# Kernel tuning notes

Measured on AMD Instinct MI355X. Metric: run time of the kernel, lower is better.

## Reference

```python
import jax, jax.numpy as jnp
import numpy as np

N_NODES = 20000
N_EDGES = 320000
N_RELS = 500
EMB = 256
D4 = EMB // 4
B = 32
GAMMA = 12.0
BN_EPS = 1e-5


def _linear(x, W, b):
    return x @ W.T + b


def _bn(x, g, b, m, v):
    # BatchNorm1d in eval mode with running stats
    return (x - m) * jax.lax.rsqrt(v + BN_EPS) * g + b


def _comp_layer(src, dst, h, e, WO, bO, WI, bI, WS, bS, bng, bnb, bnm, bnv):
    # CompGCNLayer: u_sub_e message + per-node mean over in-edges ('ho')
    # and, on the reversed graph, over out-edges ('hi'); nodes with no
    # incident edges get 0 (dgl mean semantics).
    n = h.shape[0]
    ones = jnp.ones(src.shape[0], h.dtype)
    deg_in = jnp.maximum(jax.ops.segment_sum(ones, dst, num_segments=n), 1.0)
    deg_out = jnp.maximum(jax.ops.segment_sum(ones, src, num_segments=n), 1.0)
    ho = jax.ops.segment_sum(h[src] - e, dst, num_segments=n) / deg_in[:, None]
    hi = jax.ops.segment_sum(h[dst] - e, src, num_segments=n) / deg_out[:, None]
    out = (_linear(ho, WO, bO) + _linear(hi, WI, bI) + _linear(h, WS, bS)) / 3.0
    return _bn(out, bng, bnb, bnm, bnv)


def _forward(node_embs, edge_embs, params, src, dst, e_vid, hids, rids, tids,
             is_update_g_embs, is_head_pred):
    (W_O1, b_O1, W_I1, b_I1, W_S1, b_S1, bn1_g, bn1_b, bn1_m, bn1_v, Wr1, br1,
     W_O2, b_O2, W_I2, b_I2, W_S2, b_S2, bn2_g, bn2_b, bn2_m, bn2_v, Wr2, br2) = params
    if is_update_g_embs:
        he = edge_embs[e_vid]                                   # [E, D]
        h1 = jnp.tanh(_comp_layer(src, dst, node_embs, he,
                                  W_O1, b_O1, W_I1, b_I1, W_S1, b_S1,
                                  bn1_g, bn1_b, bn1_m, bn1_v))  # [N, D/4]
        he1 = jnp.tanh(_linear(he, Wr1, br1))                   # [E, D/4]
        hn = jnp.tanh(_comp_layer(src, dst, h1, he1,
                                  W_O2, b_O2, W_I2, b_I2, W_S2, b_S2,
                                  bn2_g, bn2_b, bn2_m, bn2_v))  # [N, D]
    else:
        hn = node_embs
    heads = hn[hids]
    tails = hn[tids]
    rels = _linear(jax.nn.relu(_linear(edge_embs[rids], Wr1, br1)), Wr2, br2)
    b = hids.shape[0]
    n = hn.shape[0]
    # Faithful to torch repeat_interleave indexing in predict():
    # flat element k pairs query row k//C with candidate row k//B.
    cand_idx = (jnp.arange(b)[:, None] * n + jnp.arange(n)[None, :]) // b  # [B, N]
    cand = hn[cand_idx]                                                    # [B, N, D]
    if is_head_pred == 1:
        diff = cand + (rels - tails)[:, None, :]
    else:
        diff = (heads + rels)[:, None, :] - cand
    dist = jnp.sqrt(jnp.sum(diff * diff, axis=-1))  # p = norm = 2
    score = jax.nn.sigmoid(GAMMA - dist)
    return hn, score


def setup_inputs() -> dict:
    key = jax.random.key(0)
    ks = jax.random.split(key, 20)
    w = lambda k, shp: jax.random.normal(k, shp, jnp.float32) * 0.05
    inp = {
        "node_embs": jax.random.normal(ks[0], (N_NODES, EMB), jnp.float32),
        "edge_embs": jax.random.normal(ks[1], (N_RELS, EMB), jnp.float32),
        "W_O1": w(ks[2], (D4, EMB)), "b_O1": jnp.zeros((D4,), jnp.float32),
        "W_I1": w(ks[3], (D4, EMB)), "b_I1": jnp.zeros((D4,), jnp.float32),
        "W_S1": w(ks[4], (D4, EMB)), "b_S1": jnp.zeros((D4,), jnp.float32),
        "bn1_g": jnp.ones((D4,), jnp.float32), "bn1_b": jnp.zeros((D4,), jnp.float32),
        "bn1_m": jnp.zeros((D4,), jnp.float32), "bn1_v": jnp.ones((D4,), jnp.float32),
        "Wr1": w(ks[5], (D4, EMB)), "br1": jnp.zeros((D4,), jnp.float32),
        "W_O2": w(ks[6], (EMB, D4)), "b_O2": jnp.zeros((EMB,), jnp.float32),
        "W_I2": w(ks[7], (EMB, D4)), "b_I2": jnp.zeros((EMB,), jnp.float32),
        "W_S2": w(ks[8], (EMB, D4)), "b_S2": jnp.zeros((EMB,), jnp.float32),
        "bn2_g": jnp.ones((EMB,), jnp.float32), "bn2_b": jnp.zeros((EMB,), jnp.float32),
        "bn2_m": jnp.zeros((EMB,), jnp.float32), "bn2_v": jnp.ones((EMB,), jnp.float32),
        "Wr2": w(ks[9], (EMB, D4)), "br2": jnp.zeros((EMB,), jnp.float32),
        "src": jax.random.randint(ks[10], (N_EDGES,), 0, N_NODES, jnp.int32),
        "dst": jax.random.randint(ks[11], (N_EDGES,), 0, N_NODES, jnp.int32),
        "e_vid": jax.random.randint(ks[12], (N_EDGES,), 0, N_RELS, jnp.int32),
        "hids": jax.random.randint(ks[13], (B,), 0, N_NODES, jnp.int32),
        "rids": jax.random.randint(ks[14], (B,), 0, N_RELS, jnp.int32),
        "tids": jax.random.randint(ks[15], (B,), 0, N_NODES, jnp.int32),
        "is_update_g_embs": 1,
        "is_head_pred": 0,
    }
    return inp


def reference(node_embs, edge_embs,
              W_O1, b_O1, W_I1, b_I1, W_S1, b_S1, bn1_g, bn1_b, bn1_m, bn1_v,
              Wr1, br1,
              W_O2, b_O2, W_I2, b_I2, W_S2, b_S2, bn2_g, bn2_b, bn2_m, bn2_v,
              Wr2, br2,
              src, dst, e_vid, hids, rids, tids,
              is_update_g_embs, is_head_pred):
    params = (W_O1, b_O1, W_I1, b_I1, W_S1, b_S1, bn1_g, bn1_b, bn1_m, bn1_v,
              Wr1, br1,
              W_O2, b_O2, W_I2, b_I2, W_S2, b_S2, bn2_g, bn2_b, bn2_m, bn2_v,
              Wr2, br2)
    return _forward(node_embs, edge_embs, params, src, dst, e_vid,
                    hids, rids, tids, is_update_g_embs, is_head_pred)
```

## Files before the change

kernel.cpp:

```cpp
#include <hip/hip_runtime.h>
#include <math.h>

#define NN 20000
#define NE 320000
#define NR 500
#define EMBD 256
#define D4 64
#define BQ 32
#define TOT (2 * NN)
#define NB 40

#define NBLK_HIST 1250
#define NBLK_BN 448
#define NBLK_K1 (NBLK_HIST + NBLK_BN + 2 + BQ)

#define NBLK_GC1 939
#define NBLK_GE1 32
#define NBLK_MEGA (NBLK_GC1 + NBLK_GE1 + NBLK_HIST)

typedef __attribute__((ext_vector_type(8))) short bf16x8;
typedef __attribute__((ext_vector_type(4))) float f32x4;

__device__ __forceinline__ unsigned short f2bf(float x)
{
    unsigned int u = __float_as_uint(x);
    unsigned int r = (u + 0x7fffu + ((u >> 16) & 1u)) >> 16;
    return (unsigned short)r;
}

__device__ __forceinline__ float4 bf4tof4(uint2 u)
{
    float4 r;
    r.x = __uint_as_float((u.x & 0xFFFFu) << 16);
    r.y = __uint_as_float(u.x & 0xFFFF0000u);
    r.z = __uint_as_float((u.y & 0xFFFFu) << 16);
    r.w = __uint_as_float(u.y & 0xFFFF0000u);
    return r;
}

__global__ __launch_bounds__(256) void k_prep(
    const int* __restrict__ src, const int* __restrict__ dst,
    const int* __restrict__ evid, int* __restrict__ cnt, unsigned* __restrict__ rank2,
    const float* __restrict__ W_O1, const float* __restrict__ W_I1,
    const float* __restrict__ W_S1, const float* __restrict__ Wr1,
    const float* __restrict__ W_O2, const float* __restrict__ W_I2,
    const float* __restrict__ W_S2,
    unsigned short* __restrict__ Bn1, unsigned short* __restrict__ Bn2,
    const float* __restrict__ bO1, const float* __restrict__ bI1,
    const float* __restrict__ bS1,
    const float* __restrict__ g1, const float* __restrict__ bb1,
    const float* __restrict__ m1, const float* __restrict__ v1,
    const float* __restrict__ bO2, const float* __restrict__ bI2,
    const float* __restrict__ bS2,
    const float* __restrict__ g2, const float* __restrict__ bb2,
    const float* __restrict__ m2, const float* __restrict__ v2,
    float* __restrict__ s1, float* __restrict__ t1,
    float* __restrict__ s2, float* __restrict__ t2,
    const float* __restrict__ edge_embs,
    const float* __restrict__ br1, const float* __restrict__ br2,
    const float* __restrict__ Wr2full, const int* __restrict__ rids,
    float* __restrict__ rels)
{
    int b = blockIdx.x;
    if (b < NBLK_HIST) {
        int i = b * 256 + threadIdx.x;
        if (i < NE) {
            int r_in = atomicAdd(&cnt[dst[i]], 1);
            int r_out = atomicAdd(&cnt[NN + src[i]], 1);
            rank2[i] = (unsigned)r_in | ((unsigned)r_out << 16);
        }
        return;
    }
    b -= NBLK_HIST;
    if (b < NBLK_BN) {
        int id = b * 256 + threadIdx.x;
        if (id < 256 * 256) {
            int n = id >> 8, k = id & 255;
            float v;
            if (n < 64)       v = W_O1[n * 256 + k];
            else if (n < 128) v = W_I1[(n - 64) * 256 + k];
            else if (n < 192) v = W_S1[(n - 128) * 256 + k];
            else              v = Wr1[(n - 192) * 256 + k];
            Bn1[id] = f2bf(v);
        } else {
            int id2 = id - 256 * 256;
            if (id2 < 256 * 192) {
                int n = id2 / 192, k = id2 - n * 192;
                float v;
                if (k < 64)       v = W_O2[n * 64 + k];
                else if (k < 128) v = W_I2[n * 64 + (k - 64)];
                else              v = W_S2[n * 64 + (k - 128)];
                Bn2[id2] = f2bf(v);
            }
        }
        return;
    }
    b -= NBLK_BN;
    if (b < 2) {
        int i = b * 256 + threadIdx.x;
        if (i < 64) {
            float rsg = g1[i] / sqrtf(v1[i] + 1e-5f);
            s1[i] = rsg * (1.f / 3.f);
            t1[i] = ((bO1[i] + bI1[i] + bS1[i]) * (1.f / 3.f) - m1[i]) * rsg + bb1[i];
        } else if (i < 320) {
            int n = i - 64;
            float rsg = g2[n] / sqrtf(v2[n] + 1e-5f);
            s2[n] = rsg * (1.f / 3.f);
            t2[n] = ((bO2[n] + bI2[n] + bS2[n]) * (1.f / 3.f) - m2[n]) * rsg + bb2[n];
        }
        return;
    }
    {
        __shared__ float e_s[256];
        __shared__ float m_s[64];
        int rb = b - 2, o = threadIdx.x;
        int rid = rids[rb];
        e_s[o] = edge_embs[(size_t)rid * 256 + o];
        __syncthreads();
        if (o < 64) {
            float acc = br1[o];
            for (int k = 0; k < 256; ++k) acc = fmaf(e_s[k], Wr1[o * 256 + k], acc);
            m_s[o] = fmaxf(acc, 0.f);
        }
        __syncthreads();
        float r = br2[o];
        for (int jj = 0; jj < 64; ++jj) r = fmaf(m_s[jj], Wr2full[o * 64 + jj], r);
        rels[rb * 256 + o] = r;
    }
}


__global__ __launch_bounds__(256) void k_scanA(const int* __restrict__ cnt,
                                               int* __restrict__ bsum)
{
    __shared__ int lds[256];
    int t = threadIdx.x;
    int base = blockIdx.x * 1024 + t * 4;
    int s = 0;
    if (base + 3 < TOT) {
        int4 v = *(const int4*)(cnt + base);
        s = v.x + v.y + v.z + v.w;
    } else {
        for (int c = 0; c < 4; ++c) { int i = base + c; if (i < TOT) s += cnt[i]; }
    }
    lds[t] = s;
    __syncthreads();
    for (int d = 128; d > 0; d >>= 1) {
        if (t < d) lds[t] += lds[t + d];
        __syncthreads();
    }
    if (t == 0) bsum[blockIdx.x] = lds[0];
}

__global__ __launch_bounds__(64) void k_scanB(int* __restrict__ bsum)
{
    int t = threadIdx.x;
    int v = (t < NB) ? bsum[t] : 0;
#pragma unroll
    for (int d = 1; d < 64; d <<= 1) {
        int u = __shfl_up(v, d, 64);
        if (t >= d) v += u;
    }
    int ex = __shfl_up(v, 1, 64);
    if (t == 0) ex = 0;
    if (t < NB) bsum[t] = ex;
}

__global__ __launch_bounds__(256) void k_scanC(const int* __restrict__ cnt,
                                               const int* __restrict__ bsum,
                                               int* __restrict__ offc)
{
    __shared__ int lds[256];
    int t = threadIdx.x;
    int base = blockIdx.x * 1024 + t * 4;
    int e0 = 0, e1 = 0, e2 = 0, e3 = 0;
    if (base + 3 < TOT) {
        int4 v = *(const int4*)(cnt + base);
        e0 = v.x; e1 = v.y; e2 = v.z; e3 = v.w;
    } else {
        if (base + 0 < TOT) e0 = cnt[base + 0];
        if (base + 1 < TOT) e1 = cnt[base + 1];
        if (base + 2 < TOT) e2 = cnt[base + 2];
        if (base + 3 < TOT) e3 = cnt[base + 3];
    }
    int s = e0 + e1 + e2 + e3;
    lds[t] = s;
    __syncthreads();
    for (int d = 1; d < 256; d <<= 1) {
        int u = (t >= d) ? lds[t - d] : 0;
        __syncthreads();
        lds[t] += u;
        __syncthreads();
    }
    int run = lds[t] - s + bsum[blockIdx.x];
    if (base + 3 < TOT) {
        int4 o = make_int4(run, run + e0, run + e0 + e1, run + e0 + e1 + e2);
        *(int4*)(offc + base) = o;
    } else {
        int r = run;
        if (base + 0 < TOT) { offc[base + 0] = r; r += e0; }
        if (base + 1 < TOT) { offc[base + 1] = r; r += e1; }
        if (base + 2 < TOT) { offc[base + 2] = r; r += e2; }
        if (base + 3 < TOT) { offc[base + 3] = r; r += e3; }
    }
    if (blockIdx.x == 0 && t == 0) offc[TOT] = 2 * NE;
}

__device__ __forceinline__ void gemm_dev(
    unsigned short* As, unsigned short* Bs,
    const void* __restrict__ Av, int aBf16, int M, int K, int lda,
    const unsigned short* __restrict__ Bn,
    void* __restrict__ C, int ldc, int mode,
    const float* __restrict__ sv, const float* __restrict__ tv,
    const float* __restrict__ node_embs, const int* __restrict__ flag,
    int m0, int n0)
{
    const int t = threadIdx.x;
    const int lane = t & 63, wave = t >> 6;
    const int wr = wave >> 1, wc = wave & 1;
    const int lrow = lane & 15, lkg = lane >> 4;

    f32x4 acc[2][2] = {};

    for (int kb = 0; kb < K; kb += 64) {
        if (aBf16) {
            const unsigned short* A = (const unsigned short*)Av;
#pragma unroll
            for (int it = 0; it < 2; ++it) {
                int idx = t + it * 256;
                int ko = idx & 7;
                int row = idx >> 3;
                int gm = m0 + row;
                uint4 a = make_uint4(0u, 0u, 0u, 0u);
                if (gm < M) a = *(const uint4*)(A + (size_t)gm * lda + kb + 8 * ko);
                *(uint4*)&As[row * 72 + 8 * ko] = a;
            }
        } else {
            const float* A = (const float*)Av;
#pragma unroll
            for (int it = 0; it < 4; ++it) {
                int idx = t + it * 256;
                int kq = idx & 15;
                int row = idx >> 4;
                int gm = m0 + row;
                float4 a = make_float4(0.f, 0.f, 0.f, 0.f);
                if (gm < M) a = *(const float4*)(A + (size_t)gm * lda + kb + 4 * kq);
                unsigned int p0 = (unsigned int)f2bf(a.x) | ((unsigned int)f2bf(a.y) << 16);
                unsigned int p1 = (unsigned int)f2bf(a.z) | ((unsigned int)f2bf(a.w) << 16);
                *(uint2*)&As[row * 72 + 4 * kq] = make_uint2(p0, p1);
            }
        }
#pragma unroll
        for (int it = 0; it < 2; ++it) {
            int idx = t + it * 256;
            int ko = idx & 7;
            int row = idx >> 3;
            uint4 b = *(const uint4*)(Bn + (size_t)(n0 + row) * K + kb + 8 * ko);
            *(uint4*)&Bs[row * 72 + 8 * ko] = b;
        }
        __syncthreads();
#pragma unroll
        for (int ks = 0; ks < 2; ++ks) {
            int k0 = ks * 32 + lkg * 8;
            bf16x8 af0 = *(const bf16x8*)&As[(wr * 32 + lrow) * 72 + k0];
            bf16x8 af1 = *(const bf16x8*)&As[(wr * 32 + 16 + lrow) * 72 + k0];
            bf16x8 bf0 = *(const bf16x8*)&Bs[(wc * 32 + lrow) * 72 + k0];
            bf16x8 bf1 = *(const bf16x8*)&Bs[(wc * 32 + 16 + lrow) * 72 + k0];
            acc[0][0] = __builtin_amdgcn_mfma_f32_16x16x32_bf16(af0, bf0, acc[0][0], 0, 0, 0);
            acc[0][1] = __builtin_amdgcn_mfma_f32_16x16x32_bf16(af0, bf1, acc[0][1], 0, 0, 0);
            acc[1][0] = __builtin_amdgcn_mfma_f32_16x16x32_bf16(af1, bf0, acc[1][0], 0, 0, 0);
            acc[1][1] = __builtin_amdgcn_mfma_f32_16x16x32_bf16(af1, bf1, acc[1][1], 0, 0, 0);
        }
        __syncthreads();
    }

#pragma unroll
    for (int m = 0; m < 2; ++m) {
#pragma unroll
        for (int r = 0; r < 4; ++r) {
            int gm = m0 + wr * 32 + m * 16 + lkg * 4 + r;
            if (gm >= M) continue;
#pragma unroll
            for (int n = 0; n < 2; ++n) {
                int gn = n0 + wc * 32 + n * 16 + lrow;
                float v = acc[m][n][r];
                if (mode == 0) {
                    ((unsigned short*)C)[(size_t)gm * ldc + gn] = f2bf(v);
                } else if (mode == 1) {
                    float val = (gn >= 192) ? tanhf(v + sv[gn - 192]) : v;
                    ((unsigned short*)C)[(size_t)gm * ldc + gn] = f2bf(val);
                } else {
                    float val = tanhf(v * sv[gn] + tv[gn]);
                    if (flag[0] == 0) val = node_embs[(size_t)gm * EMBD + gn];
                    ((float*)C)[(size_t)gm * EMBD + gn] = val;
                }
            }
        }
    }
}

__global__ __launch_bounds__(256) void gemm_mfma(
    const void* __restrict__ A, int aBf16, int M, int K, int lda,
    const unsigned short* __restrict__ Bn,
    void* __restrict__ C, int ldc, int mode,
    const float* __restrict__ sv, const float* __restrict__ tv,
    const float* __restrict__ node_embs, const int* __restrict__ flag)
{
    __shared__ unsigned short As[64 * 72];
    __shared__ unsigned short Bs[64 * 72];
    gemm_dev(As, Bs, A, aBf16, M, K, lda, Bn, C, ldc, mode, sv, tv, node_embs, flag,
             blockIdx.x * 64, blockIdx.y * 64);
}

__global__ __launch_bounds__(256) void k_mega(
    const float* __restrict__ node_embs, const float* __restrict__ edge_embs,
    const unsigned short* __restrict__ Bn1,
    unsigned short* __restrict__ C1b, unsigned short* __restrict__ E1b,
    const float* __restrict__ br1,
    const int* __restrict__ src, const int* __restrict__ dst,
    const int* __restrict__ evid, const unsigned* __restrict__ rank2,
    const int* __restrict__ offc, unsigned* __restrict__ R)
{
    __shared__ unsigned short As[64 * 72];
    __shared__ unsigned short Bs[64 * 72];
    int bid = blockIdx.x;
    if (bid < NBLK_GC1) {
        gemm_dev(As, Bs, node_embs, 0, NN, 256, 256, Bn1, C1b, 192, 0,
                 nullptr, nullptr, nullptr, nullptr,
                 (bid % 313) * 64, (bid / 313) * 64);
    } else if (bid < NBLK_GC1 + NBLK_GE1) {
        int b2 = bid - NBLK_GC1;
        gemm_dev(As, Bs, edge_embs, 0, NR, 256, 256, Bn1, E1b, 256, 1,
                 br1, nullptr, nullptr, nullptr,
                 (b2 % 8) * 64, (b2 / 8) * 64);
    } else {
        int e = (bid - NBLK_GC1 - NBLK_GE1) * 256 + threadIdx.x;
        if (e < NE) {
            int s = src[e], d = dst[e];
            unsigned rv = (unsigned)evid[e] << 15;
            unsigned rk = rank2[e];
            R[offc[d] + (rk & 0xFFFFu)] = (unsigned)s | rv;
            R[offc[NN + s] + (rk >> 16)] = (unsigned)d | rv;
        }
    }
}


__device__ __forceinline__ void gather_quad(
    const unsigned* __restrict__ R, int r0, int r1, int g, int q,
    const unsigned short* __restrict__ TAB, int ldt, int toff,
    const unsigned short* __restrict__ ETAB, int eoff,
    float4& acc)
{
    int lane = g * 16 + q;
    int cnt = r1 - r0;
    for (int base = 0; base < cnt; base += 64) {
        int rem = cnt - base; if (rem > 64) rem = 64;
        unsigned rec = 0u;
        if (lane < rem) rec = R[r0 + base + lane];
        int i = 0;
        for (; 4 * i + 15 < rem; i += 4) {
            unsigned ra = __shfl(rec, 4 * i + g, 64);
            unsigned rb = __shfl(rec, 4 * i + 4 + g, 64);
            unsigned rc = __shfl(rec, 4 * i + 8 + g, 64);
            unsigned rd = __shfl(rec, 4 * i + 12 + g, 64);
            uint2 ua0 = *(const uint2*)(TAB + (size_t)(ra & 0x7FFFu) * ldt + toff + 4 * q);
            uint2 ue0 = *(const uint2*)(ETAB + (size_t)(ra >> 15) * 256 + eoff + 4 * q);
            uint2 ua1 = *(const uint2*)(TAB + (size_t)(rb & 0x7FFFu) * ldt + toff + 4 * q);
            uint2 ue1 = *(const uint2*)(ETAB + (size_t)(rb >> 15) * 256 + eoff + 4 * q);
            uint2 ua2 = *(const uint2*)(TAB + (size_t)(rc & 0x7FFFu) * ldt + toff + 4 * q);
            uint2 ue2 = *(const uint2*)(ETAB + (size_t)(rc >> 15) * 256 + eoff + 4 * q);
            uint2 ua3 = *(const uint2*)(TAB + (size_t)(rd & 0x7FFFu) * ldt + toff + 4 * q);
            uint2 ue3 = *(const uint2*)(ETAB + (size_t)(rd >> 15) * 256 + eoff + 4 * q);
            float4 a0 = bf4tof4(ua0), e0 = bf4tof4(ue0);
            float4 a1 = bf4tof4(ua1), e1 = bf4tof4(ue1);
            float4 a2 = bf4tof4(ua2), e2 = bf4tof4(ue2);
            float4 a3 = bf4tof4(ua3), e3 = bf4tof4(ue3);
            acc.x += (a0.x - e0.x) + (a1.x - e1.x) + (a2.x - e2.x) + (a3.x - e3.x);
            acc.y += (a0.y - e0.y) + (a1.y - e1.y) + (a2.y - e2.y) + (a3.y - e3.y);
            acc.z += (a0.z - e0.z) + (a1.z - e1.z) + (a2.z - e2.z) + (a3.z - e3.z);
            acc.w += (a0.w - e0.w) + (a1.w - e1.w) + (a2.w - e2.w) + (a3.w - e3.w);
        }
        for (; 4 * i < rem; ++i) {
            int idx = 4 * i + g;
            unsigned rr = __shfl(rec, idx < rem ? idx : 0, 64);
            if (idx < rem) {
                uint2 ua = *(const uint2*)(TAB + (size_t)(rr & 0x7FFFu) * ldt + toff + 4 * q);
                uint2 ue = *(const uint2*)(ETAB + (size_t)(rr >> 15) * 256 + eoff + 4 * q);
                float4 a = bf4tof4(ua), e = bf4tof4(ue);
                acc.x += a.x - e.x; acc.y += a.y - e.y;
                acc.z += a.z - e.z; acc.w += a.w - e.w;
            }
        }
    }
}

__device__ __forceinline__ void xreduce(float4& v)
{
    v.x += __shfl_xor(v.x, 16, 64); v.y += __shfl_xor(v.y, 16, 64);
    v.z += __shfl_xor(v.z, 16, 64); v.w += __shfl_xor(v.w, 16, 64);
    v.x += __shfl_xor(v.x, 32, 64); v.y += __shfl_xor(v.y, 32, 64);
    v.z += __shfl_xor(v.z, 32, 64); v.w += __shfl_xor(v.w, 32, 64);
}

__device__ __forceinline__ uint2 packbf4(float4 o)
{
    return make_uint2((unsigned)f2bf(o.x) | ((unsigned)f2bf(o.y) << 16),
                      (unsigned)f2bf(o.z) | ((unsigned)f2bf(o.w) << 16));
}

__global__ __launch_bounds__(256) void k_gather1(
    const int* __restrict__ offc, const unsigned* __restrict__ R,
    const unsigned short* __restrict__ C1b, const unsigned short* __restrict__ E1b,
    const float* __restrict__ s1, const float* __restrict__ t1,
    unsigned short* __restrict__ A2b)
{
    int n = blockIdx.x * 4 + (threadIdx.x >> 6);
    if (n >= NN) return;
    int lane = threadIdx.x & 63, g = lane >> 4, q = lane & 15;
    int b0 = offc[n], b1 = offc[n + 1];
    int c0 = offc[NN + n], c1 = offc[NN + n + 1];
    float di = 1.f / fmaxf((float)(b1 - b0), 1.f);
    float dh = 1.f / fmaxf((float)(c1 - c0), 1.f);
    float4 accO = make_float4(0.f, 0.f, 0.f, 0.f);
    float4 accI = make_float4(0.f, 0.f, 0.f, 0.f);
    gather_quad(R, b0, b1, g, q, C1b, 192, 0, E1b, 0, accO);
    gather_quad(R, c0, c1, g, q, C1b, 192, 64, E1b, 64, accI);
    xreduce(accO);
    xreduce(accI);
    if (g == 0) {
        float4 hs = bf4tof4(*(const uint2*)(C1b + (size_t)n * 192 + 128 + 4 * q));
        float4 sv = *(const float4*)(s1 + 4 * q);
        float4 tv = *(const float4*)(t1 + 4 * q);
        float4 o;
        o.x = tanhf((accO.x * di + accI.x * dh + hs.x) * sv.x + tv.x);
        o.y = tanhf((accO.y * di + accI.y * dh + hs.y) * sv.y + tv.y);
        o.z = tanhf((accO.z * di + accI.z * dh + hs.z) * sv.z + tv.z);
        o.w = tanhf((accO.w * di + accI.w * dh + hs.w) * sv.w + tv.w);
        *(uint2*)(A2b + (size_t)n * 192 + 128 + 4 * q) = packbf4(o);
    }
}

__global__ __launch_bounds__(256) void k_gather2(
    const int* __restrict__ offc, const unsigned* __restrict__ R,
    const unsigned short* __restrict__ A2r, const unsigned short* __restrict__ E1b,
    unsigned short* __restrict__ A2w)
{
    int n = blockIdx.x * 4 + (threadIdx.x >> 6);
    if (n >= NN) return;
    int lane = threadIdx.x & 63, g = lane >> 4, q = lane & 15;
    int b0 = offc[n], b1 = offc[n + 1];
    int c0 = offc[NN + n], c1 = offc[NN + n + 1];
    float di = 1.f / fmaxf((float)(b1 - b0), 1.f);
    float dh = 1.f / fmaxf((float)(c1 - c0), 1.f);
    float4 accO = make_float4(0.f, 0.f, 0.f, 0.f);
    float4 accI = make_float4(0.f, 0.f, 0.f, 0.f);
    gather_quad(R, b0, b1, g, q, A2r, 192, 128, E1b, 192, accO);
    gather_quad(R, c0, c1, g, q, A2r, 192, 128, E1b, 192, accI);
    xreduce(accO);
    xreduce(accI);
    if (g == 0) {
        float4 o0, o1;
        o0.x = accO.x * di; o0.y = accO.y * di; o0.z = accO.z * di; o0.w = accO.w * di;
        o1.x = accI.x * dh; o1.y = accI.y * dh; o1.z = accI.z * dh; o1.w = accI.w * dh;
        *(uint2*)(A2w + (size_t)n * 192 + 4 * q) = packbf4(o0);
        *(uint2*)(A2w + (size_t)n * 192 + 64 + 4 * q) = packbf4(o1);
    }
}

__global__ __launch_bounds__(256) void k_tvec(
    const float* __restrict__ rels, const float* __restrict__ hn,
    const int* __restrict__ hids, const int* __restrict__ tids,
    const int* __restrict__ is_head, float* __restrict__ tvec)
{
    int b = blockIdx.x, o = threadIdx.x;
    int ih = is_head[0];
    int nid = ih ? tids[b] : hids[b];
    float r = rels[b * 256 + o];
    float hv = hn[(size_t)nid * 256 + o];
    tvec[b * 256 + o] = ih ? (hv - r) : (hv + r);
}

__global__ __launch_bounds__(256) void k_score(
    const float* __restrict__ hn, const float* __restrict__ tvec,
    float* __restrict__ score)
{
    int p = blockIdx.x * 4 + (threadIdx.x >> 6);
    if (p >= BQ * (NN / BQ)) return;
    int l = threadIdx.x & 63;
    int b = p / (NN / BQ);
    int j = p - b * (NN / BQ);
    int idx = (b * NN + 32 * j) / BQ;
    float ssum = 0.f;
#pragma unroll
    for (int q = 0; q < 4; ++q) {
        float df = hn[(size_t)idx * 256 + l + 64 * q] - tvec[b * 256 + l + 64 * q];
        ssum = fmaf(df, df, ssum);
    }
#pragma unroll
    for (int off = 32; off >= 1; off >>= 1) ssum += __shfl_xor(ssum, off, 64);
    float dist = sqrtf(ssum);
    float sc = 1.f / (1.f + expf(dist - 12.f));
    if (l < 32) score[(size_t)b * NN + 32 * j + l] = sc;
}

extern "C" void kernel_launch(void* const* d_in, const int* in_sizes, int n_in,
                              void* d_out, int out_size, void* d_ws, size_t ws_size,
                              hipStream_t stream)
{
    const float* node_embs = (const float*)d_in[0];
    const float* edge_embs = (const float*)d_in[1];
    const float* W_O1 = (const float*)d_in[2];  const float* b_O1 = (const float*)d_in[3];
    const float* W_I1 = (const float*)d_in[4];  const float* b_I1 = (const float*)d_in[5];
    const float* W_S1 = (const float*)d_in[6];  const float* b_S1 = (const float*)d_in[7];
    const float* bn1_g = (const float*)d_in[8]; const float* bn1_b = (const float*)d_in[9];
    const float* bn1_m = (const float*)d_in[10];const float* bn1_v = (const float*)d_in[11];
    const float* Wr1 = (const float*)d_in[12];  const float* br1 = (const float*)d_in[13];
    const float* W_O2 = (const float*)d_in[14]; const float* b_O2 = (const float*)d_in[15];
    const float* W_I2 = (const float*)d_in[16]; const float* b_I2 = (const float*)d_in[17];
    const float* W_S2 = (const float*)d_in[18]; const float* b_S2 = (const float*)d_in[19];
    const float* bn2_g = (const float*)d_in[20];const float* bn2_b = (const float*)d_in[21];
    const float* bn2_m = (const float*)d_in[22];const float* bn2_v = (const float*)d_in[23];
    const float* Wr2 = (const float*)d_in[24];  const float* br2 = (const float*)d_in[25];
    const int* src = (const int*)d_in[26];
    const int* dst = (const int*)d_in[27];
    const int* evid = (const int*)d_in[28];
    const int* hids = (const int*)d_in[29];
    const int* rids = (const int*)d_in[30];
    const int* tids = (const int*)d_in[31];
    const int* upd = (const int*)d_in[32];
    const int* ihead = (const int*)d_in[33];

    unsigned short* C1b = (unsigned short*)d_ws;
    unsigned short* A2b = C1b + 3840000;
    unsigned short* E1b = A2b + 3840000;
    unsigned short* Bn1 = E1b + 128000;
    unsigned short* Bn2 = Bn1 + 65536;

    float* s1   = (float*)(Bn2 + 49152);
    float* t1   = s1 + 64;
    float* s2   = t1 + 64;
    float* t2   = s2 + 256;
    float* rels = t2 + 256;
    float* tvec = rels + 8192;

    unsigned* R     = (unsigned*)(tvec + 8192);
    unsigned* rank2 = R + 2 * NE;
    int* cnt    = (int*)(rank2 + NE);
    int* offc   = cnt + TOT;
    int* bsum   = offc + TOT + 1;

    float* hn    = (float*)d_out;
    float* score = hn + (size_t)NN * EMBD;

    hipMemsetAsync(cnt, 0, (size_t)TOT * 4, stream);

    k_prep<<<NBLK_K1, 256, 0, stream>>>(
        src, dst, evid, cnt, rank2,
        W_O1, W_I1, W_S1, Wr1, W_O2, W_I2, W_S2, Bn1, Bn2,
        b_O1, b_I1, b_S1, bn1_g, bn1_b, bn1_m, bn1_v,
        b_O2, b_I2, b_S2, bn2_g, bn2_b, bn2_m, bn2_v,
        s1, t1, s2, t2,
        edge_embs, br1, br2, Wr2, rids, rels);

    k_scanA<<<NB, 256, 0, stream>>>(cnt, bsum);
    k_scanB<<<1, 64, 0, stream>>>(bsum);
    k_scanC<<<NB, 256, 0, stream>>>(cnt, bsum, offc);

    k_mega<<<NBLK_MEGA, 256, 0, stream>>>(node_embs, edge_embs, Bn1,
                                          C1b, E1b, br1, src, dst, evid, rank2, offc, R);

    k_gather1<<<NN / 4, 256, 0, stream>>>(offc, R, C1b, E1b, s1, t1, A2b);
    k_gather2<<<NN / 4, 256, 0, stream>>>(offc, R, A2b, E1b, A2b);

    gemm_mfma<<<dim3(313, 4), 256, 0, stream>>>(A2b, 1, NN, 192, 192, Bn2,
                                                hn, 256, 2, s2, t2, node_embs, upd);

    k_tvec<<<BQ, 256, 0, stream>>>(rels, hn, hids, tids, ihead, tvec);
    k_score<<<(BQ * (NN / BQ)) / 4, 256, 0, stream>>>(hn, tvec, score);
}
```

Baseline: 143.2 us.

## Privatize edge histogram into 8 partitions and repack CSR per bin

The degree histogram now uses 8 private count arrays chosen by block index, which cuts atomic contention on shared bins. The scan is extended to produce per-partition offsets plus merged per-bin offsets. A new repack kernel copies the partitioned edge lists into one contiguous CSR array for the gather kernels. The scatter phase of k_mega is reordered to run first, and k_tvec is fused into k_score. The cost is an extra kernel, larger scans over 8x the bins, and a serial per-thread copy loop in the repack.

```diff
diff --git a/kernel.cpp b/kernel.cpp
--- a/kernel.cpp
+++ b/kernel.cpp
@@ -8,7 +8,10 @@
 #define D4 64
 #define BQ 32
 #define TOT (2 * NN)
-#define NB 40
+#define NPART 8
+#define TOT2 (NPART * TOT)
+#define NBP 313
+#define NBB 40
 
 #define NBLK_HIST 1250
 #define NBLK_BN 448
@@ -16,7 +19,7 @@
 
 #define NBLK_GC1 939
 #define NBLK_GE1 32
-#define NBLK_MEGA (NBLK_GC1 + NBLK_GE1 + NBLK_HIST)
+#define NBLK_MEGA (NBLK_HIST + NBLK_GC1 + NBLK_GE1)
 
 typedef __attribute__((ext_vector_type(8))) short bf16x8;
 typedef __attribute__((ext_vector_type(4))) float f32x4;
@@ -40,7 +43,7 @@
 
 __global__ __launch_bounds__(256) void k_prep(
     const int* __restrict__ src, const int* __restrict__ dst,
-    const int* __restrict__ evid, int* __restrict__ cnt, unsigned* __restrict__ rank2,
+    int* __restrict__ cnt2, unsigned* __restrict__ rank2,
     const float* __restrict__ W_O1, const float* __restrict__ W_I1,
     const float* __restrict__ W_S1, const float* __restrict__ Wr1,
     const float* __restrict__ W_O2, const float* __restrict__ W_I2,
@@ -64,9 +67,10 @@
     int b = blockIdx.x;
     if (b < NBLK_HIST) {
         int i = b * 256 + threadIdx.x;
+        int base = (b & (NPART - 1)) * TOT;
         if (i < NE) {
-            int r_in = atomicAdd(&cnt[dst[i]], 1);
-            int r_out = atomicAdd(&cnt[NN + src[i]], 1);
+            int r_in = atomicAdd(&cnt2[base + dst[i]], 1);
+            int r_out = atomicAdd(&cnt2[base + NN + src[i]], 1);
             rank2[i] = (unsigned)r_in | ((unsigned)r_out << 16);
         }
         return;
@@ -130,18 +134,31 @@
 }
 
 
-__global__ __launch_bounds__(256) void k_scanA(const int* __restrict__ cnt,
-                                               int* __restrict__ bsum)
+__global__ __launch_bounds__(256) void k_scanA(const int* __restrict__ cnt2,
+                                               int* __restrict__ bsum,
+                                               int* __restrict__ bsum2)
 {
     __shared__ int lds[256];
     int t = threadIdx.x;
-    int base = blockIdx.x * 1024 + t * 4;
+    int bid = blockIdx.x;
     int s = 0;
-    if (base + 3 < TOT) {
-        int4 v = *(const int4*)(cnt + base);
-        s = v.x + v.y + v.z + v.w;
+    if (bid < NBP) {
+        int base = bid * 1024 + t * 4;
+        if (base + 3 < TOT2) {
+            int4 v = *(const int4*)(cnt2 + base);
+            s = v.x + v.y + v.z + v.w;
+        } else {
+            for (int c = 0; c < 4; ++c) { int i = base + c; if (i < TOT2) s += cnt2[i]; }
+        }
     } else {
-        for (int c = 0; c < 4; ++c) { int i = base + c; if (i < TOT) s += cnt[i]; }
+        int base = (bid - NBP) * 1024 + t * 4;
+        for (int c = 0; c < 4; ++c) {
+            int bin = base + c;
+            if (bin < TOT) {
+#pragma unroll
+                for (int p = 0; p < NPART; ++p) s += cnt2[p * TOT + bin];
+            }
+        }
     }
     lds[t] = s;
     __syncthreads();
@@ -149,39 +166,66 @@
         if (t < d) lds[t] += lds[t + d];
         __syncthreads();
     }
-    if (t == 0) bsum[blockIdx.x] = lds[0];
-}
-
-__global__ __launch_bounds__(64) void k_scanB(int* __restrict__ bsum)
+    if (t == 0) {
+        if (bid < NBP) bsum[bid] = lds[0];
+        else bsum2[bid - NBP] = lds[0];
+    }
+}
+
+__global__ __launch_bounds__(64) void k_scanB(int* __restrict__ bsum, int* __restrict__ bsum2)
 {
     int t = threadIdx.x;
-    int v = (t < NB) ? bsum[t] : 0;
-#pragma unroll
-    for (int d = 1; d < 64; d <<= 1) {
-        int u = __shfl_up(v, d, 64);
-        if (t >= d) v += u;
-    }
-    int ex = __shfl_up(v, 1, 64);
-    if (t == 0) ex = 0;
-    if (t < NB) bsum[t] = ex;
-}
-
-__global__ __launch_bounds__(256) void k_scanC(const int* __restrict__ cnt,
+    int* arr = blockIdx.x ? bsum2 : bsum;
+    int nb = blockIdx.x ? NBB : NBP;
+    int carry = 0;
+    for (int c = 0; c < nb; c += 64) {
+        int i = c + t;
+        int v = (i < nb) ? arr[i] : 0;
+        int vin = v;
+#pragma unroll
+        for (int d = 1; d < 64; d <<= 1) {
+            int u = __shfl_up(v, d, 64);
+            if (t >= d) v += u;
+        }
+        if (i < nb) arr[i] = (v - vin) + carry;
+        carry += __shfl(v, 63, 64);
+    }
+}
+
+__global__ __launch_bounds__(256) void k_scanC(const int* __restrict__ cnt2,
                                                const int* __restrict__ bsum,
-                                               int* __restrict__ offc)
+                                               const int* __restrict__ bsum2,
+                                               int* __restrict__ offc2,
+                                               int* __restrict__ off_bin)
 {
     __shared__ int lds[256];
     int t = threadIdx.x;
-    int base = blockIdx.x * 1024 + t * 4;
+    int bid = blockIdx.x;
     int e0 = 0, e1 = 0, e2 = 0, e3 = 0;
-    if (base + 3 < TOT) {
-        int4 v = *(const int4*)(cnt + base);
-        e0 = v.x; e1 = v.y; e2 = v.z; e3 = v.w;
+    if (bid < NBP) {
+        int base = bid * 1024 + t * 4;
+        if (base + 3 < TOT2) {
+            int4 v = *(const int4*)(cnt2 + base);
+            e0 = v.x; e1 = v.y; e2 = v.z; e3 = v.w;
+        } else {
+            if (base + 0 < TOT2) e0 = cnt2[base + 0];
+            if (base + 1 < TOT2) e1 = cnt2[base + 1];
+            if (base + 2 < TOT2) e2 = cnt2[base + 2];
+            if (base + 3 < TOT2) e3 = cnt2[base + 3];
+        }
     } else {
-        if (base + 0 < TOT) e0 = cnt[base + 0];
-        if (base + 1 < TOT) e1 = cnt[base + 1];
-        if (base + 2 < TOT) e2 = cnt[base + 2];
-        if (base + 3 < TOT) e3 = cnt[base + 3];
+        int base = (bid - NBP) * 1024 + t * 4;
+        int es[4] = {0, 0, 0, 0};
+        for (int c = 0; c < 4; ++c) {
+            int bin = base + c;
+            if (bin < TOT) {
+                int acc = 0;
+#pragma unroll
+                for (int p = 0; p < NPART; ++p) acc += cnt2[p * TOT + bin];
+                es[c] = acc;
+            }
+        }
+        e0 = es[0]; e1 = es[1]; e2 = es[2]; e3 = es[3];
     }
     int s = e0 + e1 + e2 + e3;
     lds[t] = s;
@@ -192,18 +236,30 @@
         lds[t] += u;
         __syncthreads();
     }
-    int run = lds[t] - s + bsum[blockIdx.x];
-    if (base + 3 < TOT) {
-        int4 o = make_int4(run, run + e0, run + e0 + e1, run + e0 + e1 + e2);
-        *(int4*)(offc + base) = o;
+    if (bid < NBP) {
+        int base = bid * 1024 + t * 4;
+        int run = lds[t] - s + bsum[bid];
+        if (base + 3 < TOT2) {
+            int4 o = make_int4(run, run + e0, run + e0 + e1, run + e0 + e1 + e2);
+            *(int4*)(offc2 + base) = o;
+        } else {
+            int r = run;
+            if (base + 0 < TOT2) { offc2[base + 0] = r; r += e0; }
+            if (base + 1 < TOT2) { offc2[base + 1] = r; r += e1; }
+            if (base + 2 < TOT2) { offc2[base + 2] = r; r += e2; }
+            if (base + 3 < TOT2) { offc2[base + 3] = r; r += e3; }
+        }
+        if (bid == 0 && t == 0) offc2[TOT2] = 2 * NE;
     } else {
+        int base = (bid - NBP) * 1024 + t * 4;
+        int run = lds[t] - s + bsum2[bid - NBP];
         int r = run;
-        if (base + 0 < TOT) { offc[base + 0] = r; r += e0; }
-        if (base + 1 < TOT) { offc[base + 1] = r; r += e1; }
-        if (base + 2 < TOT) { offc[base + 2] = r; r += e2; }
-        if (base + 3 < TOT) { offc[base + 3] = r; r += e3; }
-    }
-    if (blockIdx.x == 0 && t == 0) offc[TOT] = 2 * NE;
+        if (base + 0 < TOT) { off_bin[base + 0] = r; r += e0; }
+        if (base + 1 < TOT) { off_bin[base + 1] = r; r += e1; }
+        if (base + 2 < TOT) { off_bin[base + 2] = r; r += e2; }
+        if (base + 3 < TOT) { off_bin[base + 3] = r; r += e3; }
+        if (bid == NBP && t == 0) off_bin[TOT] = 2 * NE;
+    }
 }
 
 __device__ __forceinline__ void gemm_dev(
@@ -319,29 +375,47 @@
     const float* __restrict__ br1,
     const int* __restrict__ src, const int* __restrict__ dst,
     const int* __restrict__ evid, const unsigned* __restrict__ rank2,
-    const int* __restrict__ offc, unsigned* __restrict__ R)
+    const int* __restrict__ offc2, unsigned* __restrict__ R)
 {
     __shared__ unsigned short As[64 * 72];
     __shared__ unsigned short Bs[64 * 72];
     int bid = blockIdx.x;
-    if (bid < NBLK_GC1) {
-        gemm_dev(As, Bs, node_embs, 0, NN, 256, 256, Bn1, C1b, 192, 0,
-                 nullptr, nullptr, nullptr, nullptr,
-                 (bid % 313) * 64, (bid / 313) * 64);
-    } else if (bid < NBLK_GC1 + NBLK_GE1) {
-        int b2 = bid - NBLK_GC1;
-        gemm_dev(As, Bs, edge_embs, 0, NR, 256, 256, Bn1, E1b, 256, 1,
-                 br1, nullptr, nullptr, nullptr,
-                 (b2 % 8) * 64, (b2 / 8) * 64);
-    } else {
-        int e = (bid - NBLK_GC1 - NBLK_GE1) * 256 + threadIdx.x;
+    if (bid < NBLK_HIST) {
+        int e = bid * 256 + threadIdx.x;
         if (e < NE) {
+            int base = (bid & (NPART - 1)) * TOT;
             int s = src[e], d = dst[e];
             unsigned rv = (unsigned)evid[e] << 15;
             unsigned rk = rank2[e];
-            R[offc[d] + (rk & 0xFFFFu)] = (unsigned)s | rv;
-            R[offc[NN + s] + (rk >> 16)] = (unsigned)d | rv;
-        }
+            R[offc2[base + d] + (rk & 0xFFFFu)] = (unsigned)s | rv;
+            R[offc2[base + NN + s] + (rk >> 16)] = (unsigned)d | rv;
+        }
+        return;
+    }
+    int b2 = bid - NBLK_HIST;
+    if (b2 < NBLK_GC1) {
+        gemm_dev(As, Bs, node_embs, 0, NN, 256, 256, Bn1, C1b, 192, 0,
+                 nullptr, nullptr, nullptr, nullptr,
+                 (b2 % 313) * 64, (b2 / 313) * 64);
+    } else {
+        int b3 = b2 - NBLK_GC1;
+        gemm_dev(As, Bs, edge_embs, 0, NR, 256, 256, Bn1, E1b, 256, 1,
+                 br1, nullptr, nullptr, nullptr,
+                 (b3 % 8) * 64, (b3 / 8) * 64);
+    }
+}
+
+__global__ void k_repack(const int* __restrict__ offc2, const int* __restrict__ off_bin,
+                         const unsigned* __restrict__ R, unsigned* __restrict__ R2)
+{
+    int bin = blockIdx.x * 256 + threadIdx.x;
+    if (bin >= TOT) return;
+    int d = off_bin[bin];
+#pragma unroll
+    for (int p = 0; p < NPART; ++p) {
+        int s = offc2[p * TOT + bin];
+        int e = offc2[p * TOT + bin + 1];
+        for (int i = s; i < e; ++i) R2[d++] = R[i];
     }
 }
 
@@ -410,7 +484,7 @@
 }
 
 __global__ __launch_bounds__(256) void k_gather1(
-    const int* __restrict__ offc, const unsigned* __restrict__ R,
+    const int* __restrict__ off_bin, const unsigned* __restrict__ R2,
     const unsigned short* __restrict__ C1b, const unsigned short* __restrict__ E1b,
     const float* __restrict__ s1, const float* __restrict__ t1,
     unsigned short* __restrict__ A2b)
@@ -418,14 +492,14 @@
     int n = blockIdx.x * 4 + (threadIdx.x >> 6);
     if (n >= NN) return;
     int lane = threadIdx.x & 63, g = lane >> 4, q = lane & 15;
-    int b0 = offc[n], b1 = offc[n + 1];
-    int c0 = offc[NN + n], c1 = offc[NN + n + 1];
+    int b0 = off_bin[n], b1 = off_bin[n + 1];
+    int c0 = off_bin[NN + n], c1 = off_bin[NN + n + 1];
     float di = 1.f / fmaxf((float)(b1 - b0), 1.f);
     float dh = 1.f / fmaxf((float)(c1 - c0), 1.f);
     float4 accO = make_float4(0.f, 0.f, 0.f, 0.f);
     float4 accI = make_float4(0.f, 0.f, 0.f, 0.f);
-    gather_quad(R, b0, b1, g, q, C1b, 192, 0, E1b, 0, accO);
-    gather_quad(R, c0, c1, g, q, C1b, 192, 64, E1b, 64, accI);
+    gather_quad(R2, b0, b1, g, q, C1b, 192, 0, E1b, 0, accO);
+    gather_quad(R2, c0, c1, g, q, C1b, 192, 64, E1b, 64, accI);
     xreduce(accO);
     xreduce(accI);
     if (g == 0) {
@@ -442,21 +516,21 @@
 }
 
 __global__ __launch_bounds__(256) void k_gather2(
-    const int* __restrict__ offc, const unsigned* __restrict__ R,
+    const int* __restrict__ off_bin, const unsigned* __restrict__ R2,
     const unsigned short* __restrict__ A2r, const unsigned short* __restrict__ E1b,
     unsigned short* __restrict__ A2w)
 {
     int n = blockIdx.x * 4 + (threadIdx.x >> 6);
     if (n >= NN) return;
     int lane = threadIdx.x & 63, g = lane >> 4, q = lane & 15;
-    int b0 = offc[n], b1 = offc[n + 1];
-    int c0 = offc[NN + n], c1 = offc[NN + n + 1];
+    int b0 = off_bin[n], b1 = off_bin[n + 1];
+    int c0 = off_bin[NN + n], c1 = off_bin[NN + n + 1];
     float di = 1.f / fmaxf((float)(b1 - b0), 1.f);
     float dh = 1.f / fmaxf((float)(c1 - c0), 1.f);
     float4 accO = make_float4(0.f, 0.f, 0.f, 0.f);
     float4 accI = make_float4(0.f, 0.f, 0.f, 0.f);
-    gather_quad(R, b0, b1, g, q, A2r, 192, 128, E1b, 192, accO);
-    gather_quad(R, c0, c1, g, q, A2r, 192, 128, E1b, 192, accI);
+    gather_quad(R2, b0, b1, g, q, A2r, 192, 128, E1b, 192, accO);
+    gather_quad(R2, c0, c1, g, q, A2r, 192, 128, E1b, 192, accI);
     xreduce(accO);
     xreduce(accI);
     if (g == 0) {
@@ -468,22 +542,10 @@
     }
 }
 
-__global__ __launch_bounds__(256) void k_tvec(
-    const float* __restrict__ rels, const float* __restrict__ hn,
+__global__ __launch_bounds__(256) void k_score(
+    const float* __restrict__ hn, const float* __restrict__ rels,
     const int* __restrict__ hids, const int* __restrict__ tids,
-    const int* __restrict__ is_head, float* __restrict__ tvec)
-{
-    int b = blockIdx.x, o = threadIdx.x;
-    int ih = is_head[0];
-    int nid = ih ? tids[b] : hids[b];
-    float r = rels[b * 256 + o];
-    float hv = hn[(size_t)nid * 256 + o];
-    tvec[b * 256 + o] = ih ? (hv - r) : (hv + r);
-}
-
-__global__ __launch_bounds__(256) void k_score(
-    const float* __restrict__ hn, const float* __restrict__ tvec,
-    float* __restrict__ score)
+    const int* __restrict__ is_head, float* __restrict__ score)
 {
     int p = blockIdx.x * 4 + (threadIdx.x >> 6);
     if (p >= BQ * (NN / BQ)) return;
@@ -491,10 +553,15 @@
     int b = p / (NN / BQ);
     int j = p - b * (NN / BQ);
     int idx = (b * NN + 32 * j) / BQ;
+    int ih = is_head[0];
+    int nid = ih ? tids[b] : hids[b];
     float ssum = 0.f;
 #pragma unroll
     for (int q = 0; q < 4; ++q) {
-        float df = hn[(size_t)idx * 256 + l + 64 * q] - tvec[b * 256 + l + 64 * q];
+        float r = rels[b * 256 + l + 64 * q];
+        float hv = hn[(size_t)nid * 256 + l + 64 * q];
+        float tv = ih ? (hv - r) : (hv + r);
+        float df = hn[(size_t)idx * 256 + l + 64 * q] - tv;
         ssum = fmaf(df, df, ssum);
     }
 #pragma unroll
@@ -542,40 +609,42 @@
     float* s2   = t1 + 64;
     float* t2   = s2 + 256;
     float* rels = t2 + 256;
-    float* tvec = rels + 8192;
-
-    unsigned* R     = (unsigned*)(tvec + 8192);
-    unsigned* rank2 = R + 2 * NE;
-    int* cnt    = (int*)(rank2 + NE);
-    int* offc   = cnt + TOT;
-    int* bsum   = offc + TOT + 1;
+
+    unsigned* R     = (unsigned*)(rels + 8192);
+    unsigned* R2    = R + 2 * NE;
+    unsigned* rank2 = R2 + 2 * NE;
+    int* cnt2    = (int*)(rank2 + NE);
+    int* offc2   = cnt2 + TOT2;
+    int* off_bin = offc2 + TOT2 + 1;
+    int* bsum    = off_bin + TOT + 1;
+    int* bsum2   = bsum + NBP;
 
     float* hn    = (float*)d_out;
     float* score = hn + (size_t)NN * EMBD;
 
-    hipMemsetAsync(cnt, 0, (size_t)TOT * 4, stream);
+    hipMemsetAsync(cnt2, 0, (size_t)TOT2 * 4, stream);
 
     k_prep<<<NBLK_K1, 256, 0, stream>>>(
-        src, dst, evid, cnt, rank2,
+        src, dst, cnt2, rank2,
         W_O1, W_I1, W_S1, Wr1, W_O2, W_I2, W_S2, Bn1, Bn2,
         b_O1, b_I1, b_S1, bn1_g, bn1_b, bn1_m, bn1_v,
         b_O2, b_I2, b_S2, bn2_g, bn2_b, bn2_m, bn2_v,
         s1, t1, s2, t2,
         edge_embs, br1, br2, Wr2, rids, rels);
 
-    k_scanA<<<NB, 256, 0, stream>>>(cnt, bsum);
-    k_scanB<<<1, 64, 0, stream>>>(bsum);
-    k_scanC<<<NB, 256, 0, stream>>>(cnt, bsum, offc);
+    k_scanA<<<NBP + NBB, 256, 0, stream>>>(cnt2, bsum, bsum2);
+    k_scanB<<<2, 64, 0, stream>>>(bsum, bsum2);
+    k_scanC<<<NBP + NBB, 256, 0, stream>>>(cnt2, bsum, bsum2, offc2, off_bin);
 
     k_mega<<<NBLK_MEGA, 256, 0, stream>>>(node_embs, edge_embs, Bn1,
-                                          C1b, E1b, br1, src, dst, evid, rank2, offc, R);
-
-    k_gather1<<<NN / 4, 256, 0, stream>>>(offc, R, C1b, E1b, s1, t1, A2b);
-    k_gather2<<<NN / 4, 256, 0, stream>>>(offc, R, A2b, E1b, A2b);
+                                          C1b, E1b, br1, src, dst, evid, rank2, offc2, R);
+    k_repack<<<(TOT + 255) / 256, 256, 0, stream>>>(offc2, off_bin, R, R2);
+
+    k_gather1<<<NN / 4, 256, 0, stream>>>(off_bin, R2, C1b, E1b, s1, t1, A2b);
+    k_gather2<<<NN / 4, 256, 0, stream>>>(off_bin, R2, A2b, E1b, A2b);
 
     gemm_mfma<<<dim3(313, 4), 256, 0, stream>>>(A2b, 1, NN, 192, 192, Bn2,
                                                 hn, 256, 2, s2, t2, node_embs, upd);
 
-    k_tvec<<<BQ, 256, 0, stream>>>(rels, hn, hids, tids, ihead, tvec);
-    k_score<<<(BQ * (NN / BQ)) / 4, 256, 0, stream>>>(hn, tvec, score);
-}
+    k_score<<<(BQ * (NN / BQ)) / 4, 256, 0, stream>>>(hn, rels, hids, tids, ihead, score);
+}
```

Measured after the change: 153.2 us. +7.0%, slower.

## Partition CSR scatter atomics per XCC and repack, fuse tvec into score

Applied to the files above, without the earlier changes.

The histogram pass no longer records per-edge ranks. The CSR fill now takes its slot from per-partition cursors chosen by the XCC id hardware register, writes into four overflow segments, and a new repack kernel concatenates the segments per bin. The aim is to keep atomic contention local to each XCC and to drop the rank2 buffer traffic. The cost is an extra kernel, a larger workspace and a serial per-thread copy loop. Separately, the tvec kernel is folded into k_score, which recomputes the query vector per wave.

```diff
diff --git a/kernel.cpp b/kernel.cpp
--- a/kernel.cpp
+++ b/kernel.cpp
@@ -10,13 +10,17 @@
 #define TOT (2 * NN)
 #define NB 40
 
+#define NPART 4
+#define SEG (2 * NE)
+#define XCC_HWREG 6164
+
 #define NBLK_HIST 1250
 #define NBLK_BN 448
 #define NBLK_K1 (NBLK_HIST + NBLK_BN + 2 + BQ)
 
 #define NBLK_GC1 939
 #define NBLK_GE1 32
-#define NBLK_MEGA (NBLK_GC1 + NBLK_GE1 + NBLK_HIST)
+#define NBLK_MEGA (NBLK_HIST + NBLK_GC1 + NBLK_GE1)
 
 typedef __attribute__((ext_vector_type(8))) short bf16x8;
 typedef __attribute__((ext_vector_type(4))) float f32x4;
@@ -39,8 +43,7 @@
 }
 
 __global__ __launch_bounds__(256) void k_prep(
-    const int* __restrict__ src, const int* __restrict__ dst,
-    const int* __restrict__ evid, int* __restrict__ cnt, unsigned* __restrict__ rank2,
+    const int* __restrict__ src, const int* __restrict__ dst, int* __restrict__ cnt,
     const float* __restrict__ W_O1, const float* __restrict__ W_I1,
     const float* __restrict__ W_S1, const float* __restrict__ Wr1,
     const float* __restrict__ W_O2, const float* __restrict__ W_I2,
@@ -65,9 +68,8 @@
     if (b < NBLK_HIST) {
         int i = b * 256 + threadIdx.x;
         if (i < NE) {
-            int r_in = atomicAdd(&cnt[dst[i]], 1);
-            int r_out = atomicAdd(&cnt[NN + src[i]], 1);
-            rank2[i] = (unsigned)r_in | ((unsigned)r_out << 16);
+            atomicAdd(&cnt[dst[i]], 1);
+            atomicAdd(&cnt[NN + src[i]], 1);
         }
         return;
     }
@@ -168,7 +170,7 @@
 
 __global__ __launch_bounds__(256) void k_scanC(const int* __restrict__ cnt,
                                                const int* __restrict__ bsum,
-                                               int* __restrict__ offc)
+                                               int* __restrict__ off_bin)
 {
     __shared__ int lds[256];
     int t = threadIdx.x;
@@ -195,15 +197,15 @@
     int run = lds[t] - s + bsum[blockIdx.x];
     if (base + 3 < TOT) {
         int4 o = make_int4(run, run + e0, run + e0 + e1, run + e0 + e1 + e2);
-        *(int4*)(offc + base) = o;
+        *(int4*)(off_bin + base) = o;
     } else {
         int r = run;
-        if (base + 0 < TOT) { offc[base + 0] = r; r += e0; }
-        if (base + 1 < TOT) { offc[base + 1] = r; r += e1; }
-        if (base + 2 < TOT) { offc[base + 2] = r; r += e2; }
-        if (base + 3 < TOT) { offc[base + 3] = r; r += e3; }
-    }
-    if (blockIdx.x == 0 && t == 0) offc[TOT] = 2 * NE;
+        if (base + 0 < TOT) { off_bin[base + 0] = r; r += e0; }
+        if (base + 1 < TOT) { off_bin[base + 1] = r; r += e1; }
+        if (base + 2 < TOT) { off_bin[base + 2] = r; r += e2; }
+        if (base + 3 < TOT) { off_bin[base + 3] = r; r += e3; }
+    }
+    if (blockIdx.x == 0 && t == 0) off_bin[TOT] = 2 * NE;
 }
 
 __device__ __forceinline__ void gemm_dev(
@@ -318,30 +320,52 @@
     unsigned short* __restrict__ C1b, unsigned short* __restrict__ E1b,
     const float* __restrict__ br1,
     const int* __restrict__ src, const int* __restrict__ dst,
-    const int* __restrict__ evid, const unsigned* __restrict__ rank2,
-    const int* __restrict__ offc, unsigned* __restrict__ R)
+    const int* __restrict__ evid,
+    const int* __restrict__ off_bin, int* __restrict__ cur2,
+    unsigned* __restrict__ Rov)
 {
     __shared__ unsigned short As[64 * 72];
     __shared__ unsigned short Bs[64 * 72];
     int bid = blockIdx.x;
-    if (bid < NBLK_GC1) {
+    if (bid < NBLK_HIST) {
+        int e = bid * 256 + threadIdx.x;
+        if (e < NE) {
+            int part = __builtin_amdgcn_s_getreg(XCC_HWREG) & (NPART - 1);
+            int s = src[e], d = dst[e];
+            unsigned rv = (unsigned)evid[e] << 15;
+            unsigned base = (unsigned)part * SEG;
+            int r0 = atomicAdd(&cur2[part * TOT + d], 1);
+            Rov[base + off_bin[d] + r0] = (unsigned)s | rv;
+            int r1 = atomicAdd(&cur2[part * TOT + NN + s], 1);
+            Rov[base + off_bin[NN + s] + r1] = (unsigned)d | rv;
+        }
+        return;
+    }
+    int b2 = bid - NBLK_HIST;
+    if (b2 < NBLK_GC1) {
         gemm_dev(As, Bs, node_embs, 0, NN, 256, 256, Bn1, C1b, 192, 0,
                  nullptr, nullptr, nullptr, nullptr,
-                 (bid % 313) * 64, (bid / 313) * 64);
-    } else if (bid < NBLK_GC1 + NBLK_GE1) {
-        int b2 = bid - NBLK_GC1;
+                 (b2 % 313) * 64, (b2 / 313) * 64);
+    } else {
+        int b3 = b2 - NBLK_GC1;
         gemm_dev(As, Bs, edge_embs, 0, NR, 256, 256, Bn1, E1b, 256, 1,
                  br1, nullptr, nullptr, nullptr,
-                 (b2 % 8) * 64, (b2 / 8) * 64);
-    } else {
-        int e = (bid - NBLK_GC1 - NBLK_GE1) * 256 + threadIdx.x;
-        if (e < NE) {
-            int s = src[e], d = dst[e];
-            unsigned rv = (unsigned)evid[e] << 15;
-            unsigned rk = rank2[e];
-            R[offc[d] + (rk & 0xFFFFu)] = (unsigned)s | rv;
-            R[offc[NN + s] + (rk >> 16)] = (unsigned)d | rv;
-        }
+                 (b3 % 8) * 64, (b3 / 8) * 64);
+    }
+}
+
+__global__ void k_repack(const int* __restrict__ off_bin, const int* __restrict__ cur2,
+                         const unsigned* __restrict__ Rov, unsigned* __restrict__ R2)
+{
+    int bin = blockIdx.x * 256 + threadIdx.x;
+    if (bin >= TOT) return;
+    int b0 = off_bin[bin];
+    int d = b0;
+#pragma unroll
+    for (int p = 0; p < NPART; ++p) {
+        int len = cur2[p * TOT + bin];
+        const unsigned* sp = Rov + (size_t)p * SEG + b0;
+        for (int i = 0; i < len; ++i) R2[d++] = sp[i];
     }
 }
 
@@ -410,7 +434,7 @@
 }
 
 __global__ __launch_bounds__(256) void k_gather1(
-    const int* __restrict__ offc, const unsigned* __restrict__ R,
+    const int* __restrict__ off_bin, const unsigned* __restrict__ R2,
     const unsigned short* __restrict__ C1b, const unsigned short* __restrict__ E1b,
     const float* __restrict__ s1, const float* __restrict__ t1,
     unsigned short* __restrict__ A2b)
@@ -418,14 +442,14 @@
     int n = blockIdx.x * 4 + (threadIdx.x >> 6);
     if (n >= NN) return;
     int lane = threadIdx.x & 63, g = lane >> 4, q = lane & 15;
-    int b0 = offc[n], b1 = offc[n + 1];
-    int c0 = offc[NN + n], c1 = offc[NN + n + 1];
+    int b0 = off_bin[n], b1 = off_bin[n + 1];
+    int c0 = off_bin[NN + n], c1 = off_bin[NN + n + 1];
     float di = 1.f / fmaxf((float)(b1 - b0), 1.f);
     float dh = 1.f / fmaxf((float)(c1 - c0), 1.f);
     float4 accO = make_float4(0.f, 0.f, 0.f, 0.f);
     float4 accI = make_float4(0.f, 0.f, 0.f, 0.f);
-    gather_quad(R, b0, b1, g, q, C1b, 192, 0, E1b, 0, accO);
-    gather_quad(R, c0, c1, g, q, C1b, 192, 64, E1b, 64, accI);
+    gather_quad(R2, b0, b1, g, q, C1b, 192, 0, E1b, 0, accO);
+    gather_quad(R2, c0, c1, g, q, C1b, 192, 64, E1b, 64, accI);
     xreduce(accO);
     xreduce(accI);
     if (g == 0) {
@@ -442,21 +466,21 @@
 }
 
 __global__ __launch_bounds__(256) void k_gather2(
-    const int* __restrict__ offc, const unsigned* __restrict__ R,
+    const int* __restrict__ off_bin, const unsigned* __restrict__ R2,
     const unsigned short* __restrict__ A2r, const unsigned short* __restrict__ E1b,
     unsigned short* __restrict__ A2w)
 {
     int n = blockIdx.x * 4 + (threadIdx.x >> 6);
     if (n >= NN) return;
     int lane = threadIdx.x & 63, g = lane >> 4, q = lane & 15;
-    int b0 = offc[n], b1 = offc[n + 1];
-    int c0 = offc[NN + n], c1 = offc[NN + n + 1];
+    int b0 = off_bin[n], b1 = off_bin[n + 1];
+    int c0 = off_bin[NN + n], c1 = off_bin[NN + n + 1];
     float di = 1.f / fmaxf((float)(b1 - b0), 1.f);
     float dh = 1.f / fmaxf((float)(c1 - c0), 1.f);
     float4 accO = make_float4(0.f, 0.f, 0.f, 0.f);
     float4 accI = make_float4(0.f, 0.f, 0.f, 0.f);
-    gather_quad(R, b0, b1, g, q, A2r, 192, 128, E1b, 192, accO);
-    gather_quad(R, c0, c1, g, q, A2r, 192, 128, E1b, 192, accI);
+    gather_quad(R2, b0, b1, g, q, A2r, 192, 128, E1b, 192, accO);
+    gather_quad(R2, c0, c1, g, q, A2r, 192, 128, E1b, 192, accI);
     xreduce(accO);
     xreduce(accI);
     if (g == 0) {
@@ -468,22 +492,10 @@
     }
 }
 
-__global__ __launch_bounds__(256) void k_tvec(
-    const float* __restrict__ rels, const float* __restrict__ hn,
+__global__ __launch_bounds__(256) void k_score(
+    const float* __restrict__ hn, const float* __restrict__ rels,
     const int* __restrict__ hids, const int* __restrict__ tids,
-    const int* __restrict__ is_head, float* __restrict__ tvec)
-{
-    int b = blockIdx.x, o = threadIdx.x;
-    int ih = is_head[0];
-    int nid = ih ? tids[b] : hids[b];
-    float r = rels[b * 256 + o];
-    float hv = hn[(size_t)nid * 256 + o];
-    tvec[b * 256 + o] = ih ? (hv - r) : (hv + r);
-}
-
-__global__ __launch_bounds__(256) void k_score(
-    const float* __restrict__ hn, const float* __restrict__ tvec,
-    float* __restrict__ score)
+    const int* __restrict__ is_head, float* __restrict__ score)
 {
     int p = blockIdx.x * 4 + (threadIdx.x >> 6);
     if (p >= BQ * (NN / BQ)) return;
@@ -491,10 +503,15 @@
     int b = p / (NN / BQ);
     int j = p - b * (NN / BQ);
     int idx = (b * NN + 32 * j) / BQ;
+    int ih = is_head[0];
+    int nid = ih ? tids[b] : hids[b];
     float ssum = 0.f;
 #pragma unroll
     for (int q = 0; q < 4; ++q) {
-        float df = hn[(size_t)idx * 256 + l + 64 * q] - tvec[b * 256 + l + 64 * q];
+        float r = rels[b * 256 + l + 64 * q];
+        float hv = hn[(size_t)nid * 256 + l + 64 * q];
+        float tv = ih ? (hv - r) : (hv + r);
+        float df = hn[(size_t)idx * 256 + l + 64 * q] - tv;
         ssum = fmaf(df, df, ssum);
     }
 #pragma unroll
@@ -542,21 +559,21 @@
     float* s2   = t1 + 64;
     float* t2   = s2 + 256;
     float* rels = t2 + 256;
-    float* tvec = rels + 8192;
-
-    unsigned* R     = (unsigned*)(tvec + 8192);
-    unsigned* rank2 = R + 2 * NE;
-    int* cnt    = (int*)(rank2 + NE);
-    int* offc   = cnt + TOT;
-    int* bsum   = offc + TOT + 1;
+
+    unsigned* Rov = (unsigned*)(rels + 8192);
+    unsigned* R2  = Rov + (size_t)NPART * SEG;
+    int* cur2     = (int*)(R2 + 2 * NE);
+    int* cnt      = cur2 + NPART * TOT;
+    int* off_bin  = cnt + TOT;
+    int* bsum     = off_bin + TOT + 1;
 
     float* hn    = (float*)d_out;
     float* score = hn + (size_t)NN * EMBD;
 
-    hipMemsetAsync(cnt, 0, (size_t)TOT * 4, stream);
+    hipMemsetAsync(cur2, 0, (size_t)(NPART * TOT + TOT) * 4, stream);
 
     k_prep<<<NBLK_K1, 256, 0, stream>>>(
-        src, dst, evid, cnt, rank2,
+        src, dst, cnt,
         W_O1, W_I1, W_S1, Wr1, W_O2, W_I2, W_S2, Bn1, Bn2,
         b_O1, b_I1, b_S1, bn1_g, bn1_b, bn1_m, bn1_v,
         b_O2, b_I2, b_S2, bn2_g, bn2_b, bn2_m, bn2_v,
@@ -565,17 +582,18 @@
 
     k_scanA<<<NB, 256, 0, stream>>>(cnt, bsum);
     k_scanB<<<1, 64, 0, stream>>>(bsum);
-    k_scanC<<<NB, 256, 0, stream>>>(cnt, bsum, offc);
+    k_scanC<<<NB, 256, 0, stream>>>(cnt, bsum, off_bin);
 
     k_mega<<<NBLK_MEGA, 256, 0, stream>>>(node_embs, edge_embs, Bn1,
-                                          C1b, E1b, br1, src, dst, evid, rank2, offc, R);
-
-    k_gather1<<<NN / 4, 256, 0, stream>>>(offc, R, C1b, E1b, s1, t1, A2b);
-    k_gather2<<<NN / 4, 256, 0, stream>>>(offc, R, A2b, E1b, A2b);
+                                          C1b, E1b, br1, src, dst, evid,
+                                          off_bin, cur2, Rov);
+    k_repack<<<(TOT + 255) / 256, 256, 0, stream>>>(off_bin, cur2, Rov, R2);
+
+    k_gather1<<<NN / 4, 256, 0, stream>>>(off_bin, R2, C1b, E1b, s1, t1, A2b);
+    k_gather2<<<NN / 4, 256, 0, stream>>>(off_bin, R2, A2b, E1b, A2b);
 
     gemm_mfma<<<dim3(313, 4), 256, 0, stream>>>(A2b, 1, NN, 192, 192, Bn2,
                                                 hn, 256, 2, s2, t2, node_embs, upd);
 
-    k_tvec<<<BQ, 256, 0, stream>>>(rels, hn, hids, tids, ihead, tvec);
-    k_score<<<(BQ * (NN / BQ)) / 4, 256, 0, stream>>>(hn, tvec, score);
-}
+    k_score<<<(BQ * (NN / BQ)) / 4, 256, 0, stream>>>(hn, rels, hids, tids, ihead, score);
+}
```

Result: slower. 173.7 us (+21.3%).
